# Optimization experiments

Measured on AMD Instinct MI355X. Metric: run time of the kernel, lower is better.

The kernel has to match this reference:

```python
import jax, jax.numpy as jnp
import numpy as np

FILTER_SIZE = 5
C_IN = 32
C_OUT = 64
N = 8192


def setup_inputs() -> dict:
    key = jax.random.key(0)
    k1, k2, k3 = jax.random.split(key, 3)
    L = jax.random.normal(k1, (N, N), dtype=jnp.float32) / np.float32(np.sqrt(N))
    x = jax.random.normal(k2, (C_IN, N), dtype=jnp.float32)
    theta = jax.random.normal(k3, (C_OUT, C_IN, FILTER_SIZE), dtype=jnp.float32)  # variance=1.0
    bias = jnp.zeros((C_OUT, 1), dtype=jnp.float32)
    return {"L": L, "x": x, "theta": theta, "bias": bias}


def reference(L, x, theta, bias):
    # Chebyshev recurrence vectorized over all input channels at once.
    # Original does per-channel column matvecs L @ x[c]; here T_k has shape
    # (C_in, N) and L @ x_col per channel == T @ L.T.
    T_prev = x                      # T_0, (C_in, N)
    Ts = [T_prev]
    if FILTER_SIZE > 1:
        T_curr = T_prev @ L.T       # T_1
        Ts.append(T_curr)
        for _ in range(2, FILTER_SIZE):
            T_next = 2.0 * (T_curr @ L.T) - T_prev
            Ts.append(T_next)
            T_prev, T_curr = T_curr, T_next
    X = jnp.stack(Ts, axis=-1)      # (C_in, N, K) — matches torch assemble
    y = jnp.einsum('imk,oik->om', X, theta) + bias  # (C_out, N)
    return y
```

## Files before the change

kernel.cpp:

```cpp
#include <hip/hip_runtime.h>

#define NN 8192
#define CIN 32
#define COUT 64
#define KF 5

typedef __attribute__((ext_vector_type(8))) short bf16x8_t;
typedef __attribute__((ext_vector_type(4))) float f32x4_t;

typedef const __attribute__((address_space(1))) void* as1_t;
typedef __attribute__((address_space(3))) void* as3_t;
__device__ __forceinline__ void gll16(const void* g, void* l) {
    __builtin_amdgcn_global_load_lds((as1_t)g, (as3_t)l, 16, 0, 0);
}

__device__ __forceinline__ short f2bf(float f) {
    unsigned u = __builtin_bit_cast(unsigned, f);
    unsigned r = (u + 0x7FFFu + ((u >> 16) & 1u)) >> 16;
    return (short)(unsigned short)r;
}

__device__ __forceinline__ bf16x8_t cvt8(float4 a, float4 b) {
    bf16x8_t v;
    v[0] = f2bf(a.x); v[1] = f2bf(a.y); v[2] = f2bf(a.z); v[3] = f2bf(a.w);
    v[4] = f2bf(b.x); v[5] = f2bf(b.y); v[6] = f2bf(b.z); v[7] = f2bf(b.w);
    return v;
}

__global__ void cvt_kernel(const float* __restrict__ src, short* __restrict__ dst) {
    int idx = blockIdx.x * 256 + threadIdx.x;
    float4 v = reinterpret_cast<const float4*>(src)[idx];
    short4 o;
    o.x = f2bf(v.x); o.y = f2bf(v.y); o.z = f2bf(v.z); o.w = f2bf(v.w);
    reinterpret_cast<short4*>(dst)[idx] = o;
}

__device__ __forceinline__ void stash_partials(float* red, int wave, int g, int r,
                                               const f32x4_t& acc0, const f32x4_t& acc1) {
    const int base = wave * 512 + g * 64 + r;
#pragma unroll
    for (int t = 0; t < 4; ++t) {
        red[base + t * 16]       = acc0[t];
        red[base + t * 16 + 256] = acc1[t];
    }
}

__device__ __forceinline__ float reduce8(const float* red, int tid) {
    float s = red[tid];
#pragma unroll
    for (int w = 1; w < 8; ++w) s += red[w * 512 + tid];
    return s;
}

__global__ __launch_bounds__(512, 4) void pass1_kernel(
    const float* __restrict__ L, const short* __restrict__ Tb0,
    char* __restrict__ LbC, float* __restrict__ Tf1, short* __restrict__ Tb1)
{
    __shared__ float red[4096];
    const int tid = threadIdx.x, wave = tid >> 6, lane = tid & 63;
    const int g = lane >> 4, r = lane & 15;
    const int t = blockIdx.x, i0 = t * 16;
    const int kw = wave * 1024;

    const float* Lrow = L   + (size_t)(i0 + r) * NN + kw + g * 8;
    const short* A0   = Tb0 + (size_t)r * NN        + kw + g * 8;
    const short* A1   = Tb0 + (size_t)(r + 16) * NN + kw + g * 8;
    char* LbW = LbC + (size_t)t * 262144 + wave * 32768 + lane * 16;

    f32x4_t acc0 = {0.f,0.f,0.f,0.f}, acc1 = {0.f,0.f,0.f,0.f};
    for (int it = 0; it < 32; ++it) {
        const int jl = it * 32;
        float4 l0 = *(const float4*)(Lrow + jl);
        float4 l1 = *(const float4*)(Lrow + jl + 4);
        bf16x8_t a0 = *(const bf16x8_t*)(A0 + jl);
        bf16x8_t a1 = *(const bf16x8_t*)(A1 + jl);
        bf16x8_t b = cvt8(l0, l1);
        *(bf16x8_t*)(LbW + it * 1024) = b;
        acc0 = __builtin_amdgcn_mfma_f32_16x16x32_bf16(a0, b, acc0, 0, 0, 0);
        acc1 = __builtin_amdgcn_mfma_f32_16x16x32_bf16(a1, b, acc1, 0, 0, 0);
    }

    stash_partials(red, wave, g, r, acc0, acc1);
    __syncthreads();
    const int c = tid >> 4, il = tid & 15;
    const float val = reduce8(red, tid);
    const size_t off = (size_t)c * NN + i0 + il;
    Tf1[off] = val;
    Tb1[off] = f2bf(val);
}

__device__ __forceinline__ void mid_core(const char* __restrict__ LbW,
                                         const short* __restrict__ Abase,
                                         int wave, int lane, char* stg,
                                         f32x4_t& acc0, f32x4_t& acc1)
{
    const int g = lane >> 4, r = lane & 15;
    const int kw = wave * 1024;
    const char* srcL = LbW + lane * 16;
    const short* sA0 = Abase + (size_t)(lane & 31) * NN + kw + (lane >> 5) * 8;

#pragma unroll
    for (int c0 = 0; c0 < 2; ++c0) {
        char* Ld = stg + c0 * 6144;
        char* Ad = Ld + 2048;
        gll16(srcL + c0 * 2048,        Ld);
        gll16(srcL + c0 * 2048 + 1024, Ld + 1024);
#pragma unroll
        for (int j = 0; j < 4; ++j) gll16(sA0 + c0 * 64 + j * 16, Ad + j * 1024);
    }

    for (int c = 0; c < 16; ++c) {
        if (c < 15) asm volatile("s_waitcnt vmcnt(6)" ::: "memory");
        else        asm volatile("s_waitcnt vmcnt(0)" ::: "memory");
        const char* Ld = stg + (c & 1) * 6144;
        const char* Ad = Ld + 2048;
#pragma unroll
        for (int kk = 0; kk < 2; ++kk) {
            bf16x8_t b  = *(const bf16x8_t*)(Ld + (kk * 4 + g) * 256 + r * 16);
            bf16x8_t a0 = *(const bf16x8_t*)(Ad + (kk * 4 + g) * 512 + r * 16);
            bf16x8_t a1 = *(const bf16x8_t*)(Ad + (kk * 4 + g) * 512 + 256 + r * 16);
            acc0 = __builtin_amdgcn_mfma_f32_16x16x32_bf16(a0, b, acc0, 0, 0, 0);
            acc1 = __builtin_amdgcn_mfma_f32_16x16x32_bf16(a1, b, acc1, 0, 0, 0);
        }
        if (c < 14) {
            asm volatile("s_waitcnt lgkmcnt(0)" ::: "memory");
            const int cn = c + 2;
            char* Ldn = stg + (cn & 1) * 6144;
            char* Adn = Ldn + 2048;
            gll16(srcL + cn * 2048,        Ldn);
            gll16(srcL + cn * 2048 + 1024, Ldn + 1024);
#pragma unroll
            for (int j = 0; j < 4; ++j) gll16(sA0 + cn * 64 + j * 16, Adn + j * 1024);
        }
    }
}

__global__ __launch_bounds__(512, 2) void passmid_kernel(
    const char* __restrict__ LbC, const short* __restrict__ A,
    const float* __restrict__ Tprev, float* __restrict__ Tf, short* __restrict__ Tb)
{
    __shared__ float red[4096];
    __shared__ __align__(16) char stg[8][12288];
    const int tid = threadIdx.x, wave = tid >> 6, lane = tid & 63;
    const int g = lane >> 4, r = lane & 15;
    const int t = blockIdx.x, i0 = t * 16;

    f32x4_t acc0 = {0.f,0.f,0.f,0.f}, acc1 = {0.f,0.f,0.f,0.f};
    mid_core(LbC + (size_t)t * 262144 + wave * 32768, A, wave, lane, stg[wave], acc0, acc1);

    stash_partials(red, wave, g, r, acc0, acc1);
    __syncthreads();
    const int c = tid >> 4, il = tid & 15;
    const size_t off = (size_t)c * NN + i0 + il;
    const float val = 2.0f * reduce8(red, tid) - Tprev[off];
    Tf[off] = val;
    Tb[off] = f2bf(val);
}

__global__ __launch_bounds__(512, 2) void pass4_kernel(
    const char* __restrict__ LbC, const short* __restrict__ A,
    const float* __restrict__ Tf2, const float* __restrict__ x,
    const float* __restrict__ Tf1, const float* __restrict__ Tf3,
    const float* __restrict__ theta, const float* __restrict__ bias,
    float* __restrict__ y)
{
    __shared__ float red[4096];
    __shared__ __align__(16) char stg[8][12288];
    const int tid = threadIdx.x, wave = tid >> 6, lane = tid & 63;
    const int g = lane >> 4, r = lane & 15;
    const int t = blockIdx.x, i0 = t * 16;

    f32x4_t acc0 = {0.f,0.f,0.f,0.f}, acc1 = {0.f,0.f,0.f,0.f};
    mid_core(LbC + (size_t)t * 262144 + wave * 32768, A, wave, lane, stg[wave], acc0, acc1);

    stash_partials(red, wave, g, r, acc0, acc1);
    __syncthreads();
    {
        const int c = tid >> 4, il = tid & 15;
        red[tid] = 2.0f * reduce8(red, tid) - Tf2[(size_t)c * NN + i0 + il];
    }
    __syncthreads();

    const int o = tid >> 4, il = tid & 15;
    float a0 = bias[o], a1 = bias[o + 32];
    for (int cc = 0; cc < CIN; ++cc) {
        const size_t off = (size_t)cc * NN + i0 + il;
        const float t0 = x[off], t1 = Tf1[off], t2 = Tf2[off], t3 = Tf3[off];
        const float t4 = red[cc * 16 + il];
        const float* th0 = theta + ((size_t)o * CIN + cc) * KF;
        const float* th1 = theta + ((size_t)(o + 32) * CIN + cc) * KF;
        a0 += t0 * th0[0] + t1 * th0[1] + t2 * th0[2] + t3 * th0[3] + t4 * th0[4];
        a1 += t0 * th1[0] + t1 * th1[1] + t2 * th1[2] + t3 * th1[3] + t4 * th1[4];
    }
    y[(size_t)o * NN + i0 + il]        = a0;
    y[(size_t)(o + 32) * NN + i0 + il] = a1;
}

extern "C" void kernel_launch(void* const* d_in, const int* in_sizes, int n_in,
                              void* d_out, int out_size, void* d_ws, size_t ws_size,
                              hipStream_t stream) {
    const float* L     = (const float*)d_in[0];
    const float* x     = (const float*)d_in[1];
    const float* theta = (const float*)d_in[2];
    const float* bias  = (const float*)d_in[3];
    float* y = (float*)d_out;

    const size_t TE = (size_t)CIN * NN;
    const size_t LE = (size_t)NN * NN;

    char*  LbC = (char*)d_ws;
    float* Tf1 = (float*)(LbC + LE * 2);
    float* Tf2 = Tf1 + TE;
    float* Tf3 = Tf2 + TE;
    short* Tb0 = (short*)(Tf3 + TE);
    short* Tb1 = Tb0 + TE;
    short* Tb2 = Tb1 + TE;
    short* Tb3 = Tb2 + TE;

    cvt_kernel<<<256, 256, 0, stream>>>(x, Tb0);
    pass1_kernel<<<NN / 16, 512, 0, stream>>>(L, Tb0, LbC, Tf1, Tb1);
    passmid_kernel<<<NN / 16, 512, 0, stream>>>(LbC, Tb1, x,   Tf2, Tb2);
    passmid_kernel<<<NN / 16, 512, 0, stream>>>(LbC, Tb2, Tf1, Tf3, Tb3);
    pass4_kernel<<<NN / 16, 512, 0, stream>>>(LbC, Tb3, Tf2, x, Tf1, Tf3,
                                              theta, bias, y);
}
```

Baseline: 248.6 us.

## Split pass1 reduction dimension across two blocks with separate combine kernel

Pass1 now launches twice as many blocks, each handling half of the K dimension of the row stripe. Partial results go to a new workspace buffer, and a separate combine kernel adds the halves and writes the fp32 and bf16 T1. The change also switches the L reads to nontemporal loads and raises the occupancy hint in launch bounds. It aims to increase parallelism and memory-level concurrency for the bandwidth-bound streaming of L, at the cost of an extra kernel launch and an extra partial-buffer round trip.

```diff
diff --git a/kernel.cpp b/kernel.cpp
--- a/kernel.cpp
+++ b/kernel.cpp
@@ -20,10 +20,10 @@
     return (short)(unsigned short)r;
 }
 
-__device__ __forceinline__ bf16x8_t cvt8(float4 a, float4 b) {
+__device__ __forceinline__ bf16x8_t cvt8v(f32x4_t a, f32x4_t b) {
     bf16x8_t v;
-    v[0] = f2bf(a.x); v[1] = f2bf(a.y); v[2] = f2bf(a.z); v[3] = f2bf(a.w);
-    v[4] = f2bf(b.x); v[5] = f2bf(b.y); v[6] = f2bf(b.z); v[7] = f2bf(b.w);
+    v[0] = f2bf(a[0]); v[1] = f2bf(a[1]); v[2] = f2bf(a[2]); v[3] = f2bf(a[3]);
+    v[4] = f2bf(b[0]); v[5] = f2bf(b[1]); v[6] = f2bf(b[2]); v[7] = f2bf(b[3]);
     return v;
 }
 
@@ -52,29 +52,31 @@
     return s;
 }
 
-__global__ __launch_bounds__(512, 4) void pass1_kernel(
+__global__ __launch_bounds__(512, 8) void pass1_kernel(
     const float* __restrict__ L, const short* __restrict__ Tb0,
-    char* __restrict__ LbC, float* __restrict__ Tf1, short* __restrict__ Tb1)
+    char* __restrict__ LbC, float* __restrict__ part)
 {
     __shared__ float red[4096];
     const int tid = threadIdx.x, wave = tid >> 6, lane = tid & 63;
     const int g = lane >> 4, r = lane & 15;
-    const int t = blockIdx.x, i0 = t * 16;
-    const int kw = wave * 1024;
+    const int t = blockIdx.x >> 1, h = blockIdx.x & 1;
+    const int i0 = t * 16;
+    const int kw = h * 4096 + wave * 512;
 
     const float* Lrow = L   + (size_t)(i0 + r) * NN + kw + g * 8;
     const short* A0   = Tb0 + (size_t)r * NN        + kw + g * 8;
     const short* A1   = Tb0 + (size_t)(r + 16) * NN + kw + g * 8;
-    char* LbW = LbC + (size_t)t * 262144 + wave * 32768 + lane * 16;
+    char* LbW = LbC + (size_t)t * 262144 + (size_t)(h * 4 + (wave >> 1)) * 32768
+              + (wave & 1) * 16384 + lane * 16;
 
     f32x4_t acc0 = {0.f,0.f,0.f,0.f}, acc1 = {0.f,0.f,0.f,0.f};
-    for (int it = 0; it < 32; ++it) {
+    for (int it = 0; it < 16; ++it) {
         const int jl = it * 32;
-        float4 l0 = *(const float4*)(Lrow + jl);
-        float4 l1 = *(const float4*)(Lrow + jl + 4);
+        f32x4_t l0 = __builtin_nontemporal_load(reinterpret_cast<const f32x4_t*>(Lrow + jl));
+        f32x4_t l1 = __builtin_nontemporal_load(reinterpret_cast<const f32x4_t*>(Lrow + jl) + 1);
         bf16x8_t a0 = *(const bf16x8_t*)(A0 + jl);
         bf16x8_t a1 = *(const bf16x8_t*)(A1 + jl);
-        bf16x8_t b = cvt8(l0, l1);
+        bf16x8_t b = cvt8v(l0, l1);
         *(bf16x8_t*)(LbW + it * 1024) = b;
         acc0 = __builtin_amdgcn_mfma_f32_16x16x32_bf16(a0, b, acc0, 0, 0, 0);
         acc1 = __builtin_amdgcn_mfma_f32_16x16x32_bf16(a1, b, acc1, 0, 0, 0);
@@ -83,10 +85,21 @@
     stash_partials(red, wave, g, r, acc0, acc1);
     __syncthreads();
     const int c = tid >> 4, il = tid & 15;
-    const float val = reduce8(red, tid);
-    const size_t off = (size_t)c * NN + i0 + il;
-    Tf1[off] = val;
-    Tb1[off] = f2bf(val);
+    part[(size_t)h * CIN * NN + (size_t)c * NN + i0 + il] = reduce8(red, tid);
+}
+
+__global__ __launch_bounds__(256) void combine1_kernel(
+    const float* __restrict__ part, float* __restrict__ Tf1, short* __restrict__ Tb1)
+{
+    const int idx = blockIdx.x * 256 + threadIdx.x;
+    const float4 p0 = reinterpret_cast<const float4*>(part)[idx];
+    const float4 p1 = reinterpret_cast<const float4*>(part + (size_t)CIN * NN)[idx];
+    float4 v;
+    v.x = p0.x + p1.x; v.y = p0.y + p1.y; v.z = p0.z + p1.z; v.w = p0.w + p1.w;
+    reinterpret_cast<float4*>(Tf1)[idx] = v;
+    short4 b;
+    b.x = f2bf(v.x); b.y = f2bf(v.y); b.z = f2bf(v.z); b.w = f2bf(v.w);
+    reinterpret_cast<short4*>(Tb1)[idx] = b;
 }
 
 __device__ __forceinline__ void mid_core(const char* __restrict__ LbW,
@@ -216,9 +229,11 @@
     short* Tb1 = Tb0 + TE;
     short* Tb2 = Tb1 + TE;
     short* Tb3 = Tb2 + TE;
+    float* part = (float*)(Tb3 + TE);
 
     cvt_kernel<<<256, 256, 0, stream>>>(x, Tb0);
-    pass1_kernel<<<NN / 16, 512, 0, stream>>>(L, Tb0, LbC, Tf1, Tb1);
+    pass1_kernel<<<NN / 8, 512, 0, stream>>>(L, Tb0, LbC, part);
+    combine1_kernel<<<256, 256, 0, stream>>>(part, Tf1, Tb1);
     passmid_kernel<<<NN / 16, 512, 0, stream>>>(LbC, Tb1, x,   Tf2, Tb2);
     passmid_kernel<<<NN / 16, 512, 0, stream>>>(LbC, Tb2, Tf1, Tf3, Tb3);
     pass4_kernel<<<NN / 16, 512, 0, stream>>>(LbC, Tb3, Tf2, x, Tf1, Tf3,
```

After: 242.7 us. 1.02x faster.
